# Kernel tuning notes

Hardware: AMD Instinct MI355X
Metric: run time of the kernel (lower is better)

Reference implementation:

```python
import jax, jax.numpy as jnp
import numpy as np

B, TQ, TK, F, H = 8, 2048, 2048, 1024, 1024


def setup_inputs() -> dict:
    key = jax.random.key(0)
    ks = jax.random.split(key, 9)
    scale = 1.0 / np.sqrt(F)
    query = jax.random.normal(ks[0], (B, TQ, F), dtype=jnp.float32)
    encoder_states = jax.random.normal(ks[1], (B, TK, F), dtype=jnp.float32)
    # boolean attention mask; True = keep. Random Bernoulli(0.5).
    target_mask = jax.random.randint(ks[2], (B, TQ, TK), 0, 2) > 0
    # Linear params (torch nn.Linear: y = x @ W.T + b); store W as [F, H] for x @ W.
    Wq = jax.random.normal(ks[3], (F, H), dtype=jnp.float32) * scale
    bq = jax.random.normal(ks[4], (H,), dtype=jnp.float32) * scale
    Wk = jax.random.normal(ks[5], (F, H), dtype=jnp.float32) * scale
    bk = jax.random.normal(ks[6], (H,), dtype=jnp.float32) * scale
    Wv = jax.random.normal(ks[7], (F, H), dtype=jnp.float32) * scale
    bv = jax.random.normal(ks[8], (H,), dtype=jnp.float32) * scale
    return {"query": query, "encoder_states": encoder_states, "target_mask": target_mask,
            "Wq": Wq, "bq": bq, "Wk": Wk, "bk": bk, "Wv": Wv, "bv": bv}


def reference(query, encoder_states, target_mask, Wq, bq, Wk, bk, Wv, bv):
    # init(): K/V projections of encoder states
    K = jnp.einsum('btf,fh->bth', encoder_states, Wk) + bk   # [B,TK,H]
    V = jnp.einsum('btf,fh->bth', encoder_states, Wv) + bv   # [B,TK,H]
    # forward()
    Q = jnp.einsum('btf,fh->bth', query, Wq) + bq            # [B,TQ,H]
    scores = jnp.einsum('bqh,bkh->bqk', Q, K) / jnp.sqrt(jnp.asarray(H, Q.dtype))
    scores = jnp.where(target_mask, scores, -jnp.inf)
    attn = jax.nn.softmax(scores, axis=-1)                   # [B,TQ,TK]
    return jnp.einsum('bqk,bkh->bqh', attn, V)               # [B,TQ,H]
```

## Files before the change

kernel.cpp:

```cpp
#include <hip/hip_runtime.h>

#define NB 8
#define TQv 2048
#define TKv 2048
#define FD 1024
#define HD 1024

typedef __attribute__((ext_vector_type(8))) short short8;
typedef __attribute__((ext_vector_type(8))) _Float16 half8;
typedef __attribute__((ext_vector_type(16))) float f32x16;

__device__ __forceinline__ short f2bf(float f) {
    union { float f; unsigned u; } v; v.f = f;
    unsigned r = v.u + 0x7FFFu + ((v.u >> 16) & 1u);
    return (short)(r >> 16);
}

__device__ __forceinline__ void async16(const short* g, short* l) {
    __builtin_amdgcn_global_load_lds(
        (const __attribute__((address_space(1))) unsigned int*)g,
        (__attribute__((address_space(3))) unsigned int*)l, 16, 0, 0);
}

template <bool F16>
__device__ __forceinline__ void gemm128_core(const short* __restrict__ A, int lda,
                                             const short* __restrict__ B, int ldb,
                                             int K, short* As, short* Bs,
                                             f32x16 acc[2][2], int tid) {
    int wave = tid >> 6, lane = tid & 63;
    int lr = lane >> 3;
    int kc = (lane & 7) ^ lr;
    const short* ga[4]; const short* gb[4];
    short* la[4]; short* lb[4];
#pragma unroll
    for (int j = 0; j < 4; ++j) {
        int w = wave + 4 * j;
        ga[j] = A + (size_t)(8 * w + lr) * lda + kc * 8;
        gb[j] = B + (size_t)(8 * w + lr) * ldb + kc * 8;
        la[j] = As + w * 512;
        lb[j] = Bs + w * 512;
    }
    int mbase = (wave & 1) * 64 + (lane & 31);
    int nbase = (wave >> 1) * 64 + (lane & 31);
    int khalf = lane >> 5;
    int l7 = lane & 7;

    for (int k0 = 0; k0 < K; k0 += 64) {
        __syncthreads();
#pragma unroll
        for (int j = 0; j < 4; ++j) { async16(ga[j], la[j]); async16(gb[j], lb[j]); }
#pragma unroll
        for (int j = 0; j < 4; ++j) { ga[j] += 64; gb[j] += 64; }
        __syncthreads();
#pragma unroll
        for (int ks = 0; ks < 4; ++ks) {
            int kcc = 2 * ks + khalf;
            int sw = kcc ^ l7;
            if (F16) {
                half8 af[2], bf[2];
#pragma unroll
                for (int mt = 0; mt < 2; ++mt) {
                    af[mt] = *(const half8*)(As + ((mbase + mt * 32) * 8 + sw) * 8);
                    bf[mt] = *(const half8*)(Bs + ((nbase + mt * 32) * 8 + sw) * 8);
                }
#pragma unroll
                for (int mt = 0; mt < 2; ++mt)
#pragma unroll
                    for (int nt = 0; nt < 2; ++nt)
                        acc[mt][nt] = __builtin_amdgcn_mfma_f32_32x32x16_f16(
                            af[mt], bf[nt], acc[mt][nt], 0, 0, 0);
            } else {
                short8 af[2], bf[2];
#pragma unroll
                for (int mt = 0; mt < 2; ++mt) {
                    af[mt] = *(const short8*)(As + ((mbase + mt * 32) * 8 + sw) * 8);
                    bf[mt] = *(const short8*)(Bs + ((nbase + mt * 32) * 8 + sw) * 8);
                }
#pragma unroll
                for (int mt = 0; mt < 2; ++mt)
#pragma unroll
                    for (int nt = 0; nt < 2; ++nt)
                        acc[mt][nt] = __builtin_amdgcn_mfma_f32_32x32x16_bf16(
                            af[mt], bf[nt], acc[mt][nt], 0, 0, 0);
            }
        }
    }
}
#define ACC0 {0.f,0.f,0.f,0.f,0.f,0.f,0.f,0.f,0.f,0.f,0.f,0.f,0.f,0.f,0.f,0.f}
#define ACC_INIT {{ACC0, ACC0}, {ACC0, ACC0}}
#define EPI_GM(mt, r) (tile_m + (wave & 1) * 64 + (mt) * 32 + ((lane >> 5) << 2) + (((r) >> 2) << 3) + ((r) & 3))
#define EPI_GN(nt)    (tile_n + (wave >> 1) * 64 + (nt) * 32 + (lane & 31))

__global__ __launch_bounds__(256) void convert_kernel(const float* __restrict__ q,
                                                      const float* __restrict__ e,
                                                      short* __restrict__ xq,
                                                      short* __restrict__ xe) {
    size_t i = (size_t)blockIdx.x * 256 + threadIdx.x;
    const float* src = blockIdx.y ? e : q;
    short* dst = blockIdx.y ? xe : xq;
    float4 a = ((const float4*)src)[2 * i];
    float4 b = ((const float4*)src)[2 * i + 1];
    short8 v;
    v[0] = f2bf(a.x); v[1] = f2bf(a.y); v[2] = f2bf(a.z); v[3] = f2bf(a.w);
    v[4] = f2bf(b.x); v[5] = f2bf(b.y); v[6] = f2bf(b.z); v[7] = f2bf(b.w);
    ((short8*)dst)[i] = v;
}

__global__ __launch_bounds__(256) void wtrans_kernel(const float* __restrict__ Wq,
                                                     const float* __restrict__ Wk,
                                                     const float* __restrict__ Wv,
                                                     short* __restrict__ Wt) {
    __shared__ float tile[32][33];
    const float* W = (blockIdx.z == 0) ? Wq : (blockIdx.z == 1) ? Wk : Wv;
    short* dst = Wt + (size_t)blockIdx.z * HD * FD;
    int h0 = blockIdx.x * 32, f0 = blockIdx.y * 32;
    int tx = threadIdx.x, ty = threadIdx.y;
    for (int j = ty; j < 32; j += 8)
        tile[j][tx] = W[(size_t)(f0 + j) * HD + h0 + tx];
    __syncthreads();
    for (int j = ty; j < 32; j += 8)
        dst[(size_t)(h0 + j) * FD + f0 + tx] = f2bf(tile[tx][j]);
}

__global__ __launch_bounds__(256, 4) void projqk_kernel(const short* __restrict__ Xq,
                                                        const short* __restrict__ Xe,
                                                        const short* __restrict__ Wt3,
                                                        const float* __restrict__ bq,
                                                        const float* __restrict__ bk,
                                                        short* __restrict__ Q,
                                                        short* __restrict__ K) {
    __shared__ short As[128 * 64];
    __shared__ short Bs[128 * 64];
    int tid = threadIdx.x;
    int wave = tid >> 6, lane = tid & 63;
    int p = blockIdx.z;
    const short* X = (p == 0) ? Xq : Xe;
    const short* Wt = Wt3 + (size_t)p * HD * FD;
    const float* bias = (p == 0) ? bq : bk;
    short* O = (p == 0) ? Q : K;
    int bid = blockIdx.x;
    int xcd = bid & 7;
    int idx = bid >> 3;
    int n_t = idx & 7;
    int m_t = (idx >> 3) * 8 + xcd;
    int tile_m = m_t * 128;
    int tile_n = n_t * 128;
    f32x16 acc[2][2] = ACC_INIT;
    gemm128_core<false>(X + (size_t)tile_m * FD, FD, Wt + (size_t)tile_n * FD, FD, FD,
                        As, Bs, acc, tid);
#pragma unroll
    for (int nt = 0; nt < 2; ++nt) {
        int gn = EPI_GN(nt);
        float bv_ = bias[gn];
#pragma unroll
        for (int mt = 0; mt < 2; ++mt)
#pragma unroll
            for (int r = 0; r < 16; ++r) {
                int gm = EPI_GM(mt, r);
                O[(size_t)gm * HD + gn] = f2bf(acc[mt][nt][r] + bv_);
            }
    }
}

__global__ __launch_bounds__(256, 4) void projv_kernel(const short* __restrict__ Xe,
                                                       const short* __restrict__ Wtv,
                                                       const float* __restrict__ bv,
                                                       short* __restrict__ Vt) {
    __shared__ short As[128 * 64];
    __shared__ short Bs[128 * 64];
    int tid = threadIdx.x;
    int wave = tid >> 6, lane = tid & 63;
    int id = blockIdx.x;
    int b = id & 7;
    int i = id >> 3;
    int n_t = i & 15;
    int m_t = i >> 4;
    int tile_m = m_t * 128;
    int tile_n = n_t * 128;
    const short* Xb = Xe + (size_t)b * TKv * FD;
    f32x16 acc[2][2] = ACC_INIT;
    gemm128_core<false>(Wtv + (size_t)tile_m * FD, FD, Xb + (size_t)tile_n * FD, FD, FD,
                        As, Bs, acc, tid);
    short* Ob = Vt + (size_t)b * HD * TKv;
#pragma unroll
    for (int mt = 0; mt < 2; ++mt)
#pragma unroll
        for (int r = 0; r < 16; ++r) {
            int gm = EPI_GM(mt, r);
            float bv_ = bv[gm];
#pragma unroll
            for (int nt = 0; nt < 2; ++nt) {
                int gn = EPI_GN(nt);
                union { _Float16 h; short s; } cv;
                cv.h = (_Float16)(acc[mt][nt][r] + bv_);
                Ob[(size_t)gm * TKv + gn] = cv.s;
            }
        }
}

__global__ __launch_bounds__(256) void maskbits_kernel(const int* __restrict__ mask,
                                                       unsigned long long* __restrict__ Mbits,
                                                       float* __restrict__ L) {
    int tid = threadIdx.x;
    int lane = tid & 63;
    if (blockIdx.x < 64) L[blockIdx.x * 256 + tid] = 0.f;
    const int NW = NB * TQv * (TKv / 64);
    int stride = gridDim.x * 4;
    for (int w = blockIdx.x * 4 + (tid >> 6); w < NW; w += stride) {
        int v = mask[(size_t)w * 64 + lane];
        unsigned long long bal = __ballot(v != 0);
        if (lane == 0) Mbits[w] = bal;
    }
}

__global__ __launch_bounds__(256, 4) void score_kernel(const short* __restrict__ Q,
                                                       const short* __restrict__ K,
                                                       const unsigned long long* __restrict__ Mbits,
                                                       short* __restrict__ S,
                                                       float* __restrict__ L) {
    __shared__ short As[128 * 64];
    __shared__ short Bs[128 * 64];
    int tid = threadIdx.x;
    int wave = tid >> 6, lane = tid & 63;
    int id = blockIdx.x;
    int b = id & 7;
    int i = id >> 3;
    int n_t = i & 15;
    int m_t = i >> 4;
    int tile_m = m_t * 128;
    int tile_n = n_t * 128;
    const short* Aq = Q + (size_t)b * TQv * HD;
    const short* Bk = K + (size_t)b * TKv * HD;
    f32x16 acc[2][2] = ACC_INIT;
    gemm128_core<false>(Aq + (size_t)tile_m * HD, HD, Bk + (size_t)tile_n * HD, HD, HD,
                        As, Bs, acc, tid);
    short* Sb = S + (size_t)b * TQv * TKv;
    const unsigned long long* Mb = Mbits + (size_t)b * TQv * (TKv / 64);
    float* Lb = L + (size_t)b * TQv;
    int wofs = (tile_n >> 6) + (wave >> 1);
    int l31 = lane & 31;
#pragma unroll
    for (int mt = 0; mt < 2; ++mt)
#pragma unroll
        for (int r = 0; r < 16; ++r) {
            int gm = EPI_GM(mt, r);
            unsigned long long bits = Mb[(size_t)gm * (TKv / 64) + wofs];
            float rs = 0.f;
#pragma unroll
            for (int nt = 0; nt < 2; ++nt) {
                int gn = EPI_GN(nt);
                float s = acc[mt][nt][r] * 0.03125f;
                float p = ((bits >> (nt * 32 + l31)) & 1ULL)
                              ? exp2f((s - 4.0f) * 1.44269504f) : 0.f;
                rs += p;
                union { _Float16 h; short sh; } cv;
                cv.h = (_Float16)p;
                Sb[(size_t)gm * TKv + gn] = cv.sh;
            }
            for (int sh = 1; sh < 32; sh <<= 1) rs += __shfl_xor(rs, sh);
            if (l31 == 0) atomicAdd(&Lb[gm], rs);
        }
}

__global__ __launch_bounds__(256, 4) void pv_kernel(const short* __restrict__ P,
                                                    const short* __restrict__ Vt,
                                                    const float* __restrict__ L,
                                                    float* __restrict__ Out) {
    __shared__ short As[128 * 64];
    __shared__ short Bs[128 * 64];
    int tid = threadIdx.x;
    int wave = tid >> 6, lane = tid & 63;
    int id = blockIdx.x;
    int b = id & 7;
    int i = id >> 3;
    int n_t = i & 7;
    int m_t = i >> 3;
    int tile_m = m_t * 128;
    int tile_n = n_t * 128;
    const short* Ap = P + (size_t)b * TQv * TKv;
    const short* Bv = Vt + (size_t)b * HD * TKv;
    const float* Lb = L + (size_t)b * TQv;
    f32x16 acc[2][2] = ACC_INIT;
    gemm128_core<true>(Ap + (size_t)tile_m * TKv, TKv, Bv + (size_t)tile_n * TKv, TKv, TKv,
                       As, Bs, acc, tid);
    float* Ob = Out + (size_t)b * TQv * HD;
#pragma unroll
    for (int mt = 0; mt < 2; ++mt)
#pragma unroll
        for (int r = 0; r < 16; ++r) {
            int gm = EPI_GM(mt, r);
            float l = Lb[gm];
            float inv = (l > 0.f) ? 1.f / l : 0.f;
#pragma unroll
            for (int nt = 0; nt < 2; ++nt) {
                int gn = EPI_GN(nt);
                Ob[(size_t)gm * HD + gn] = acc[mt][nt][r] * inv;
            }
        }
}

extern "C" void kernel_launch(void* const* d_in, const int* in_sizes, int n_in,
                              void* d_out, int out_size, void* d_ws, size_t ws_size,
                              hipStream_t stream) {
    const float* query = (const float*)d_in[0];
    const float* enc   = (const float*)d_in[1];
    const int*   mask  = (const int*)d_in[2];
    const float* Wq    = (const float*)d_in[3];
    const float* bq    = (const float*)d_in[4];
    const float* Wk    = (const float*)d_in[5];
    const float* bk    = (const float*)d_in[6];
    const float* Wv    = (const float*)d_in[7];
    const float* bv    = (const float*)d_in[8];
    float* out = (float*)d_out;

    char* ws = (char*)d_ws;
    short* Wt  = (short*)(ws);
    unsigned long long* Mbits = (unsigned long long*)(ws);
    float* L   = (float*)(ws + 4194304);
    short* Xq  = (short*)(ws + 6291456);
    short* Xe  = (short*)(ws + 39845888);
    short* S   = (short*)(ws + 6291456);
    short* Qb  = (short*)(ws + 73400320);
    short* Kb  = (short*)(ws + 106954752);
    short* Vt  = (short*)(ws + 140509184);
    (void)in_sizes; (void)n_in; (void)out_size; (void)ws_size;

    convert_kernel<<<dim3(8192, 2), 256, 0, stream>>>(query, enc, Xq, Xe);
    wtrans_kernel<<<dim3(32, 32, 3), dim3(32, 8), 0, stream>>>(Wq, Wk, Wv, Wt);
    projqk_kernel<<<dim3(1024, 1, 2), 256, 0, stream>>>(Xq, Xe, Wt, bq, bk, Qb, Kb);
    projv_kernel<<<dim3(1024), 256, 0, stream>>>(Xe, Wt + (size_t)2 * HD * FD, bv, Vt);
    maskbits_kernel<<<dim3(2048), 256, 0, stream>>>(mask, Mbits, L);
    score_kernel<<<dim3(2048), 256, 0, stream>>>(Qb, Kb, Mbits, S, L);
    pv_kernel<<<dim3(1024), 256, 0, stream>>>(S, Vt, L, out);
}
```

Before: 636.5 us.

## Replace 128x128 GEMM core with double-buffered 256x256 tile pipeline using 16x16 MFMA

Every GEMM (Q/K/V projections, scores, PV) now uses a 256x256 output tile computed by 8 waves. The inputs are double-buffered in 128KB of dynamic LDS and prefetched with async global-to-LDS loads interleaved among 16x16x32 MFMA groups. Explicit vmcnt/lgkmcnt waits, barriers and setprio control the schedule. This raises data reuse per block and overlaps loads with math, at the cost of fewer blocks (one or two per CU given the LDS use), higher register pressure and strict reliance on hand-placed waits.

```diff
diff --git a/kernel.cpp b/kernel.cpp
--- a/kernel.cpp
+++ b/kernel.cpp
@@ -8,7 +8,7 @@
 
 typedef __attribute__((ext_vector_type(8))) short short8;
 typedef __attribute__((ext_vector_type(8))) _Float16 half8;
-typedef __attribute__((ext_vector_type(16))) float f32x16;
+typedef __attribute__((ext_vector_type(4))) float f32x4;
 
 __device__ __forceinline__ short f2bf(float f) {
     union { float f; unsigned u; } v; v.f = f;
@@ -16,80 +16,114 @@
     return (short)(r >> 16);
 }
 
+__device__ __forceinline__ half8 as_h8(short8 v) {
+    union { short8 s; half8 h; } u; u.s = v; return u.h;
+}
+
 __device__ __forceinline__ void async16(const short* g, short* l) {
     __builtin_amdgcn_global_load_lds(
         (const __attribute__((address_space(1))) unsigned int*)g,
         (__attribute__((address_space(3))) unsigned int*)l, 16, 0, 0);
 }
 
+#define BAR  __builtin_amdgcn_s_barrier()
+#define SP1  __builtin_amdgcn_s_setprio(1)
+#define SP0  __builtin_amdgcn_s_setprio(0)
+#define VMCNT(N) asm volatile("s_waitcnt vmcnt(" #N ")" ::: "memory")
+#define LGK0 do { asm volatile("s_waitcnt lgkmcnt(0)" ::: "memory"); \
+                  __builtin_amdgcn_sched_barrier(0); } while (0)
+
+
+#define STG_A(BF, H, T) { async16(gA[H][0] + (T)*64, lA[BF][H][0]); \
+                          async16(gA[H][1] + (T)*64, lA[BF][H][1]); }
+#define STG_B(BF, H, T) { async16(gB[H][0] + (T)*64, lB[BF][H][0]); \
+                          async16(gB[H][1] + (T)*64, lB[BF][H][1]); }
+
+#define RD_A(dst, BF, QM) { _Pragma("unroll") for (int ml = 0; ml < 4; ++ml) { \
+    dst[ml][0] = *(const short8*)(rdA + (BF)*65536 + ((QM)*64 + ml*16)*128 + o0); \
+    dst[ml][1] = *(const short8*)(rdA + (BF)*65536 + ((QM)*64 + ml*16)*128 + o1); } }
+#define RD_B(dst, BF, QN) { _Pragma("unroll") for (int nq = 0; nq < 2; ++nq) { \
+    dst[nq][0] = *(const short8*)(rdB + (BF)*65536 + ((QN)*32 + nq*16)*128 + o0); \
+    dst[nq][1] = *(const short8*)(rdB + (BF)*65536 + ((QN)*32 + nq*16)*128 + o1); } }
+
+#define DO_MFMA(AF, BFR, QM, QN) { \
+    _Pragma("unroll") for (int ks = 0; ks < 2; ++ks) \
+    _Pragma("unroll") for (int ml = 0; ml < 4; ++ml) \
+    _Pragma("unroll") for (int nq = 0; nq < 2; ++nq) { \
+        if constexpr (F16) \
+            acc[(QM)*4 + ml][(QN)*2 + nq] = __builtin_amdgcn_mfma_f32_16x16x32_f16( \
+                as_h8(AF[ml][ks]), as_h8(BFR[nq][ks]), acc[(QM)*4 + ml][(QN)*2 + nq], 0, 0, 0); \
+        else \
+            acc[(QM)*4 + ml][(QN)*2 + nq] = __builtin_amdgcn_mfma_f32_16x16x32_bf16( \
+                AF[ml][ks], BFR[nq][ks], acc[(QM)*4 + ml][(QN)*2 + nq], 0, 0, 0); } }
+
 template <bool F16>
-__device__ __forceinline__ void gemm128_core(const short* __restrict__ A, int lda,
-                                             const short* __restrict__ B, int ldb,
-                                             int K, short* As, short* Bs,
-                                             f32x16 acc[2][2], int tid) {
-    int wave = tid >> 6, lane = tid & 63;
-    int lr = lane >> 3;
-    int kc = (lane & 7) ^ lr;
-    const short* ga[4]; const short* gb[4];
-    short* la[4]; short* lb[4];
-#pragma unroll
-    for (int j = 0; j < 4; ++j) {
-        int w = wave + 4 * j;
-        ga[j] = A + (size_t)(8 * w + lr) * lda + kc * 8;
-        gb[j] = B + (size_t)(8 * w + lr) * ldb + kc * 8;
-        la[j] = As + w * 512;
-        lb[j] = Bs + w * 512;
-    }
-    int mbase = (wave & 1) * 64 + (lane & 31);
-    int nbase = (wave >> 1) * 64 + (lane & 31);
-    int khalf = lane >> 5;
-    int l7 = lane & 7;
-
-    for (int k0 = 0; k0 < K; k0 += 64) {
-        __syncthreads();
-#pragma unroll
-        for (int j = 0; j < 4; ++j) { async16(ga[j], la[j]); async16(gb[j], lb[j]); }
-#pragma unroll
-        for (int j = 0; j < 4; ++j) { ga[j] += 64; gb[j] += 64; }
-        __syncthreads();
-#pragma unroll
-        for (int ks = 0; ks < 4; ++ks) {
-            int kcc = 2 * ks + khalf;
-            int sw = kcc ^ l7;
-            if (F16) {
-                half8 af[2], bf[2];
-#pragma unroll
-                for (int mt = 0; mt < 2; ++mt) {
-                    af[mt] = *(const half8*)(As + ((mbase + mt * 32) * 8 + sw) * 8);
-                    bf[mt] = *(const half8*)(Bs + ((nbase + mt * 32) * 8 + sw) * 8);
-                }
-#pragma unroll
-                for (int mt = 0; mt < 2; ++mt)
-#pragma unroll
-                    for (int nt = 0; nt < 2; ++nt)
-                        acc[mt][nt] = __builtin_amdgcn_mfma_f32_32x32x16_f16(
-                            af[mt], bf[nt], acc[mt][nt], 0, 0, 0);
-            } else {
-                short8 af[2], bf[2];
-#pragma unroll
-                for (int mt = 0; mt < 2; ++mt) {
-                    af[mt] = *(const short8*)(As + ((mbase + mt * 32) * 8 + sw) * 8);
-                    bf[mt] = *(const short8*)(Bs + ((nbase + mt * 32) * 8 + sw) * 8);
-                }
-#pragma unroll
-                for (int mt = 0; mt < 2; ++mt)
-#pragma unroll
-                    for (int nt = 0; nt < 2; ++nt)
-                        acc[mt][nt] = __builtin_amdgcn_mfma_f32_32x32x16_bf16(
-                            af[mt], bf[nt], acc[mt][nt], 0, 0, 0);
+__device__ __forceinline__ void gemm256_core(const short* __restrict__ A,
+                                             const short* __restrict__ B,
+                                             int ldK, int K, char* smem,
+                                             f32x4 acc[8][4], int tid) {
+    const int wid = tid >> 6, lane = tid & 63;
+    const int wm = wid >> 2, wn = wid & 3;
+
+    const int lr  = wid * 8 + (lane >> 3);
+    const int kc8 = ((lane & 7) ^ (lane >> 3)) * 8;
+    const short* gA[2][2]; const short* gB[2][2];
+    short* lA[2][2][2]; short* lB[2][2][2];
+#pragma unroll
+    for (int h = 0; h < 2; ++h)
+#pragma unroll
+        for (int j = 0; j < 2; ++j) {
+            gA[h][j] = A + (size_t)(h * 128 + j * 64 + lr) * ldK + kc8;
+            gB[h][j] = B + (size_t)(h * 128 + j * 64 + lr) * ldK + kc8;
+#pragma unroll
+            for (int bf = 0; bf < 2; ++bf) {
+                lA[bf][h][j] = (short*)(smem + bf * 65536 +         h * 16384 + (j * 512 + wid * 64) * 16);
+                lB[bf][h][j] = (short*)(smem + bf * 65536 + 32768 + h * 16384 + (j * 512 + wid * 64) * 16);
             }
         }
+
+    const int l15 = lane & 15;
+    const int o0 = (((lane >> 4)    ) ^ (lane & 7)) * 16;
+    const int o1 = (((lane >> 4) + 4) ^ (lane & 7)) * 16;
+    char* rdA = smem + wm * 16384 + l15 * 128;
+    char* rdB = smem + 32768 + (wn >> 1) * 16384 + (wn & 1) * 8192 + l15 * 128;
+
+    STG_A(0, 0, 0); STG_A(0, 1, 0); STG_B(0, 0, 0); STG_B(0, 1, 0);
+    STG_A(1, 0, 1); STG_A(1, 1, 1);
+    VMCNT(4);
+    BAR;
+
+    const int nt = K >> 6;
+    const int niter = nt >> 1;
+    short8 a0[4][2], a1[4][2], b0[2][2], b1[2][2];
+    for (int it = 0; it < niter; ++it) {
+        const int a = it * 2;
+        const bool nolast = (it != niter - 1);
+        RD_A(a0, 0, 0); RD_B(b0, 0, 0);
+        STG_B(1, 0, a + 1);
+        BAR; LGK0; SP1; DO_MFMA(a0, b0, 0, 0); SP0; BAR;
+        RD_A(a1, 0, 1);
+        STG_B(1, 1, a + 1);
+        BAR; LGK0; SP1; DO_MFMA(a1, b0, 1, 0); SP0; BAR;
+        RD_B(b1, 0, 1);
+        if (nolast) STG_A(0, 0, a + 2);
+        BAR; LGK0; SP1; DO_MFMA(a0, b1, 0, 1); SP0; BAR;
+        if (nolast) { STG_A(0, 1, a + 2); VMCNT(4); } else { VMCNT(0); }
+        BAR; SP1; DO_MFMA(a1, b1, 1, 1); SP0; BAR;
+        RD_A(a0, 1, 0); RD_B(b0, 1, 0);
+        if (nolast) STG_B(0, 0, a + 2);
+        BAR; LGK0; SP1; DO_MFMA(a0, b0, 0, 0); SP0; BAR;
+        RD_A(a1, 1, 1);
+        if (nolast) STG_B(0, 1, a + 2);
+        BAR; LGK0; SP1; DO_MFMA(a1, b0, 1, 0); SP0; BAR;
+        RD_B(b1, 1, 1);
+        if (nolast) STG_A(1, 0, a + 3);
+        BAR; LGK0; SP1; DO_MFMA(a0, b1, 0, 1); SP0; BAR;
+        if (nolast) { STG_A(1, 1, a + 3); VMCNT(4); }
+        BAR; SP1; DO_MFMA(a1, b1, 1, 1); SP0; BAR;
     }
 }
-#define ACC0 {0.f,0.f,0.f,0.f,0.f,0.f,0.f,0.f,0.f,0.f,0.f,0.f,0.f,0.f,0.f,0.f}
-#define ACC_INIT {{ACC0, ACC0}, {ACC0, ACC0}}
-#define EPI_GM(mt, r) (tile_m + (wave & 1) * 64 + (mt) * 32 + ((lane >> 5) << 2) + (((r) >> 2) << 3) + ((r) & 3))
-#define EPI_GN(nt)    (tile_n + (wave >> 1) * 64 + (nt) * 32 + (lane & 31))
+
 
 __global__ __launch_bounds__(256) void convert_kernel(const float* __restrict__ q,
                                                       const float* __restrict__ e,
@@ -122,78 +156,71 @@
         dst[(size_t)(h0 + j) * FD + f0 + tx] = f2bf(tile[tx][j]);
 }
 
-__global__ __launch_bounds__(256, 4) void projqk_kernel(const short* __restrict__ Xq,
+__global__ __launch_bounds__(512, 2) void projqk_kernel(const short* __restrict__ Xq,
                                                         const short* __restrict__ Xe,
                                                         const short* __restrict__ Wt3,
                                                         const float* __restrict__ bq,
                                                         const float* __restrict__ bk,
                                                         short* __restrict__ Q,
                                                         short* __restrict__ K) {
-    __shared__ short As[128 * 64];
-    __shared__ short Bs[128 * 64];
-    int tid = threadIdx.x;
-    int wave = tid >> 6, lane = tid & 63;
+    extern __shared__ char smem[];
+    int tid = threadIdx.x;
     int p = blockIdx.z;
-    const short* X = (p == 0) ? Xq : Xe;
+    const short* X = p ? Xe : Xq;
     const short* Wt = Wt3 + (size_t)p * HD * FD;
-    const float* bias = (p == 0) ? bq : bk;
-    short* O = (p == 0) ? Q : K;
+    const float* bias = p ? bk : bq;
+    short* O = p ? K : Q;
     int bid = blockIdx.x;
-    int xcd = bid & 7;
-    int idx = bid >> 3;
-    int n_t = idx & 7;
-    int m_t = (idx >> 3) * 8 + xcd;
-    int tile_m = m_t * 128;
-    int tile_n = n_t * 128;
-    f32x16 acc[2][2] = ACC_INIT;
-    gemm128_core<false>(X + (size_t)tile_m * FD, FD, Wt + (size_t)tile_n * FD, FD, FD,
-                        As, Bs, acc, tid);
-#pragma unroll
-    for (int nt = 0; nt < 2; ++nt) {
-        int gn = EPI_GN(nt);
+    int xcd = bid & 7, idx = bid >> 3;
+    int n_t = idx & 3, m_t = (idx >> 2) * 8 + xcd;
+    int tile_m = m_t * 256, tile_n = n_t * 256;
+    f32x4 acc[8][4] = {};
+    gemm256_core<false>(X + (size_t)tile_m * FD, Wt + (size_t)tile_n * FD, FD, FD, smem, acc, tid);
+    int wid = tid >> 6, lane = tid & 63;
+    int wm = wid >> 2, wn = wid & 3;
+    int row0 = tile_m + wm * 128 + ((lane >> 4) << 2);
+    int col0 = tile_n + wn * 64 + (lane & 15);
+#pragma unroll
+    for (int n = 0; n < 4; ++n) {
+        int gn = col0 + n * 16;
         float bv_ = bias[gn];
 #pragma unroll
-        for (int mt = 0; mt < 2; ++mt)
-#pragma unroll
-            for (int r = 0; r < 16; ++r) {
-                int gm = EPI_GM(mt, r);
-                O[(size_t)gm * HD + gn] = f2bf(acc[mt][nt][r] + bv_);
-            }
+        for (int m = 0; m < 8; ++m)
+#pragma unroll
+            for (int r = 0; r < 4; ++r)
+                O[(size_t)(row0 + m * 16 + r) * HD + gn] = f2bf(acc[m][n][r] + bv_);
     }
 }
 
-__global__ __launch_bounds__(256, 4) void projv_kernel(const short* __restrict__ Xe,
+__global__ __launch_bounds__(512, 2) void projv_kernel(const short* __restrict__ Xe,
                                                        const short* __restrict__ Wtv,
                                                        const float* __restrict__ bv,
                                                        short* __restrict__ Vt) {
-    __shared__ short As[128 * 64];
-    __shared__ short Bs[128 * 64];
-    int tid = threadIdx.x;
-    int wave = tid >> 6, lane = tid & 63;
-    int id = blockIdx.x;
-    int b = id & 7;
-    int i = id >> 3;
-    int n_t = i & 15;
-    int m_t = i >> 4;
-    int tile_m = m_t * 128;
-    int tile_n = n_t * 128;
+    extern __shared__ char smem[];
+    int tid = threadIdx.x;
+    int bid = blockIdx.x;
+    int b = bid & 7, i = bid >> 3;
+    int m_t = i & 3, n_t = i >> 2;
+    int tile_m = m_t * 256, tile_n = n_t * 256;
     const short* Xb = Xe + (size_t)b * TKv * FD;
-    f32x16 acc[2][2] = ACC_INIT;
-    gemm128_core<false>(Wtv + (size_t)tile_m * FD, FD, Xb + (size_t)tile_n * FD, FD, FD,
-                        As, Bs, acc, tid);
+    f32x4 acc[8][4] = {};
+    gemm256_core<false>(Wtv + (size_t)tile_m * FD, Xb + (size_t)tile_n * FD, FD, FD, smem, acc, tid);
     short* Ob = Vt + (size_t)b * HD * TKv;
-#pragma unroll
-    for (int mt = 0; mt < 2; ++mt)
-#pragma unroll
-        for (int r = 0; r < 16; ++r) {
-            int gm = EPI_GM(mt, r);
+    int wid = tid >> 6, lane = tid & 63;
+    int wm = wid >> 2, wn = wid & 3;
+    int row0 = tile_m + wm * 128 + ((lane >> 4) << 2);
+    int col0 = tile_n + wn * 64 + (lane & 15);
+#pragma unroll
+    for (int m = 0; m < 8; ++m)
+#pragma unroll
+        for (int r = 0; r < 4; ++r) {
+            int gm = row0 + m * 16 + r;
             float bv_ = bv[gm];
 #pragma unroll
-            for (int nt = 0; nt < 2; ++nt) {
-                int gn = EPI_GN(nt);
+            for (int n = 0; n < 4; ++n) {
                 union { _Float16 h; short s; } cv;
-                cv.h = (_Float16)(acc[mt][nt][r] + bv_);
-                Ob[(size_t)gm * TKv + gn] = cv.s;
+                cv.h = (_Float16)(acc[m][n][r] + bv_);
+                Ob[(size_t)gm * TKv + col0 + n * 16] = cv.s;
             }
         }
 }
@@ -213,89 +240,82 @@
     }
 }
 
-__global__ __launch_bounds__(256, 4) void score_kernel(const short* __restrict__ Q,
+__global__ __launch_bounds__(512, 2) void score_kernel(const short* __restrict__ Q,
                                                        const short* __restrict__ K,
                                                        const unsigned long long* __restrict__ Mbits,
                                                        short* __restrict__ S,
                                                        float* __restrict__ L) {
-    __shared__ short As[128 * 64];
-    __shared__ short Bs[128 * 64];
-    int tid = threadIdx.x;
-    int wave = tid >> 6, lane = tid & 63;
-    int id = blockIdx.x;
-    int b = id & 7;
-    int i = id >> 3;
-    int n_t = i & 15;
-    int m_t = i >> 4;
-    int tile_m = m_t * 128;
-    int tile_n = n_t * 128;
+    extern __shared__ char smem[];
+    int tid = threadIdx.x;
+    int bid = blockIdx.x;
+    int b = bid & 7, i = bid >> 3;
+    int n_t = i & 7, m_t = i >> 3;
+    int tile_m = m_t * 256, tile_n = n_t * 256;
     const short* Aq = Q + (size_t)b * TQv * HD;
     const short* Bk = K + (size_t)b * TKv * HD;
-    f32x16 acc[2][2] = ACC_INIT;
-    gemm128_core<false>(Aq + (size_t)tile_m * HD, HD, Bk + (size_t)tile_n * HD, HD, HD,
-                        As, Bs, acc, tid);
+    f32x4 acc[8][4] = {};
+    gemm256_core<false>(Aq + (size_t)tile_m * HD, Bk + (size_t)tile_n * HD, HD, HD, smem, acc, tid);
     short* Sb = S + (size_t)b * TQv * TKv;
     const unsigned long long* Mb = Mbits + (size_t)b * TQv * (TKv / 64);
     float* Lb = L + (size_t)b * TQv;
-    int wofs = (tile_n >> 6) + (wave >> 1);
-    int l31 = lane & 31;
-#pragma unroll
-    for (int mt = 0; mt < 2; ++mt)
-#pragma unroll
-        for (int r = 0; r < 16; ++r) {
-            int gm = EPI_GM(mt, r);
-            unsigned long long bits = Mb[(size_t)gm * (TKv / 64) + wofs];
+    int wid = tid >> 6, lane = tid & 63;
+    int wm = wid >> 2, wn = wid & 3;
+    int l15 = lane & 15;
+    int row0 = tile_m + wm * 128 + ((lane >> 4) << 2);
+    int col0 = tile_n + wn * 64 + l15;
+    int word = (tile_n + wn * 64) >> 6;
+#pragma unroll
+    for (int m = 0; m < 8; ++m)
+#pragma unroll
+        for (int r = 0; r < 4; ++r) {
+            int gm = row0 + m * 16 + r;
+            unsigned long long bits = Mb[(size_t)gm * (TKv / 64) + word];
             float rs = 0.f;
 #pragma unroll
-            for (int nt = 0; nt < 2; ++nt) {
-                int gn = EPI_GN(nt);
-                float s = acc[mt][nt][r] * 0.03125f;
-                float p = ((bits >> (nt * 32 + l31)) & 1ULL)
-                              ? exp2f((s - 4.0f) * 1.44269504f) : 0.f;
-                rs += p;
+            for (int n = 0; n < 4; ++n) {
+                float s = acc[m][n][r] * 0.03125f;
+                float pv = ((bits >> (n * 16 + l15)) & 1ULL)
+                               ? exp2f((s - 4.0f) * 1.44269504f) : 0.f;
+                rs += pv;
                 union { _Float16 h; short sh; } cv;
-                cv.h = (_Float16)p;
-                Sb[(size_t)gm * TKv + gn] = cv.sh;
+                cv.h = (_Float16)pv;
+                Sb[(size_t)gm * TKv + col0 + n * 16] = cv.sh;
             }
-            for (int sh = 1; sh < 32; sh <<= 1) rs += __shfl_xor(rs, sh);
-            if (l31 == 0) atomicAdd(&Lb[gm], rs);
+            for (int sh = 1; sh < 16; sh <<= 1) rs += __shfl_xor(rs, sh);
+            if (l15 == 0) atomicAdd(&Lb[gm], rs);
         }
 }
 
-__global__ __launch_bounds__(256, 4) void pv_kernel(const short* __restrict__ P,
+__global__ __launch_bounds__(512, 2) void pv_kernel(const short* __restrict__ P,
                                                     const short* __restrict__ Vt,
                                                     const float* __restrict__ L,
                                                     float* __restrict__ Out) {
-    __shared__ short As[128 * 64];
-    __shared__ short Bs[128 * 64];
-    int tid = threadIdx.x;
-    int wave = tid >> 6, lane = tid & 63;
-    int id = blockIdx.x;
-    int b = id & 7;
-    int i = id >> 3;
-    int n_t = i & 7;
-    int m_t = i >> 3;
-    int tile_m = m_t * 128;
-    int tile_n = n_t * 128;
+    extern __shared__ char smem[];
+    int tid = threadIdx.x;
+    int bid = blockIdx.x;
+    int b = bid & 7, i = bid >> 3;
+    int n_t = i & 3, m_t = i >> 2;
+    int tile_m = m_t * 256, tile_n = n_t * 256;
     const short* Ap = P + (size_t)b * TQv * TKv;
     const short* Bv = Vt + (size_t)b * HD * TKv;
     const float* Lb = L + (size_t)b * TQv;
-    f32x16 acc[2][2] = ACC_INIT;
-    gemm128_core<true>(Ap + (size_t)tile_m * TKv, TKv, Bv + (size_t)tile_n * TKv, TKv, TKv,
-                       As, Bs, acc, tid);
+    f32x4 acc[8][4] = {};
+    gemm256_core<true>(Ap + (size_t)tile_m * TKv, Bv + (size_t)tile_n * TKv, TKv, TKv, smem, acc, tid);
     float* Ob = Out + (size_t)b * TQv * HD;
-#pragma unroll
-    for (int mt = 0; mt < 2; ++mt)
-#pragma unroll
-        for (int r = 0; r < 16; ++r) {
-            int gm = EPI_GM(mt, r);
+    int wid = tid >> 6, lane = tid & 63;
+    int wm = wid >> 2, wn = wid & 3;
+    int row0 = tile_m + wm * 128 + ((lane >> 4) << 2);
+    int col0 = tile_n + wn * 64 + (lane & 15);
+#pragma unroll
+    for (int m = 0; m < 8; ++m)
+#pragma unroll
+        for (int r = 0; r < 4; ++r) {
+            int gm = row0 + m * 16 + r;
             float l = Lb[gm];
             float inv = (l > 0.f) ? 1.f / l : 0.f;
 #pragma unroll
-            for (int nt = 0; nt < 2; ++nt) {
-                int gn = EPI_GN(nt);
-                Ob[(size_t)gm * HD + gn] = acc[mt][nt][r] * inv;
-            }
+            for (int n = 0; n < 4; ++n)
+                Ob[(size_t)gm * HD + col0 + n * 16] = acc[m][n][r] * inv;
         }
 }
 
@@ -325,11 +345,20 @@
     short* Vt  = (short*)(ws + 140509184);
     (void)in_sizes; (void)n_in; (void)out_size; (void)ws_size;
 
+    static bool inited = false;
+    if (!inited) {
+        hipFuncSetAttribute((const void*)projqk_kernel, hipFuncAttributeMaxDynamicSharedMemorySize, 131072);
+        hipFuncSetAttribute((const void*)projv_kernel,  hipFuncAttributeMaxDynamicSharedMemorySize, 131072);
+        hipFuncSetAttribute((const void*)score_kernel,  hipFuncAttributeMaxDynamicSharedMemorySize, 131072);
+        hipFuncSetAttribute((const void*)pv_kernel,     hipFuncAttributeMaxDynamicSharedMemorySize, 131072);
+        inited = true;
+    }
+
     convert_kernel<<<dim3(8192, 2), 256, 0, stream>>>(query, enc, Xq, Xe);
     wtrans_kernel<<<dim3(32, 32, 3), dim3(32, 8), 0, stream>>>(Wq, Wk, Wv, Wt);
-    projqk_kernel<<<dim3(1024, 1, 2), 256, 0, stream>>>(Xq, Xe, Wt, bq, bk, Qb, Kb);
-    projv_kernel<<<dim3(1024), 256, 0, stream>>>(Xe, Wt + (size_t)2 * HD * FD, bv, Vt);
+    projqk_kernel<<<dim3(256, 1, 2), 512, 131072, stream>>>(Xq, Xe, Wt, bq, bk, Qb, Kb);
+    projv_kernel<<<dim3(256), 512, 131072, stream>>>(Xe, Wt + (size_t)2 * HD * FD, bv, Vt);
     maskbits_kernel<<<dim3(2048), 256, 0, stream>>>(mask, Mbits, L);
-    score_kernel<<<dim3(2048), 256, 0, stream>>>(Qb, Kb, Mbits, S, L);
-    pv_kernel<<<dim3(1024), 256, 0, stream>>>(S, Vt, L, out);
-}
+    score_kernel<<<dim3(512), 512, 131072, stream>>>(Qb, Kb, Mbits, S, L);
+    pv_kernel<<<dim3(256), 512, 131072, stream>>>(S, Vt, L, out);
+}
```

Result: slower. 777.3 us (+22.1%).

## Switch GEMM core from 32x32x16 to 16x16x32 MFMA tiles

Applied to the files above, without the earlier changes.

Each wave's 64x64 sub-tile is now computed with a 4x4 grid of 16x16x32 MFMAs instead of a 2x2 grid of 32x32x16 MFMAs. LDS fragment addressing and every kernel's epilogue row/column mapping are redone to match, and the score kernel's row-sum reduction now spans 16 lanes. Occupancy hints drop from 4 to 3 blocks per SM, presumably to leave room for more registers. The intent is better MFMA throughput or LDS read efficiency, at the cost of more MFMA instructions per k-step and possibly higher register pressure.

```diff
diff --git a/kernel.cpp b/kernel.cpp
--- a/kernel.cpp
+++ b/kernel.cpp
@@ -8,7 +8,7 @@
 
 typedef __attribute__((ext_vector_type(8))) short short8;
 typedef __attribute__((ext_vector_type(8))) _Float16 half8;
-typedef __attribute__((ext_vector_type(16))) float f32x16;
+typedef __attribute__((ext_vector_type(4))) float f32x4;
 
 __device__ __forceinline__ short f2bf(float f) {
     union { float f; unsigned u; } v; v.f = f;
@@ -16,6 +16,10 @@
     return (short)(r >> 16);
 }
 
+__device__ __forceinline__ half8 as_h8(short8 v) {
+    union { short8 s; half8 h; } u; u.s = v; return u.h;
+}
+
 __device__ __forceinline__ void async16(const short* g, short* l) {
     __builtin_amdgcn_global_load_lds(
         (const __attribute__((address_space(1))) unsigned int*)g,
@@ -26,7 +30,7 @@
 __device__ __forceinline__ void gemm128_core(const short* __restrict__ A, int lda,
                                              const short* __restrict__ B, int ldb,
                                              int K, short* As, short* Bs,
-                                             f32x16 acc[2][2], int tid) {
+                                             f32x4 acc[4][4], int tid) {
     int wave = tid >> 6, lane = tid & 63;
     int lr = lane >> 3;
     int kc = (lane & 7) ^ lr;
@@ -40,10 +44,13 @@
         la[j] = As + w * 512;
         lb[j] = Bs + w * 512;
     }
-    int mbase = (wave & 1) * 64 + (lane & 31);
-    int nbase = (wave >> 1) * 64 + (lane & 31);
-    int khalf = lane >> 5;
-    int l7 = lane & 7;
+    int l15 = lane & 15;
+    int g4 = lane >> 4;
+    int r7 = l15 & 7;
+    const short* aB = As + ((wave & 1) * 64 + l15) * 64;
+    const short* bB = Bs + ((wave >> 1) * 64 + l15) * 64;
+    int o0 = ((g4    ) ^ r7) * 8;
+    int o1 = ((g4 + 4) ^ r7) * 8;
 
     for (int k0 = 0; k0 < K; k0 += 64) {
         __syncthreads();
@@ -53,43 +60,31 @@
         for (int j = 0; j < 4; ++j) { ga[j] += 64; gb[j] += 64; }
         __syncthreads();
 #pragma unroll
-        for (int ks = 0; ks < 4; ++ks) {
-            int kcc = 2 * ks + khalf;
-            int sw = kcc ^ l7;
-            if (F16) {
-                half8 af[2], bf[2];
-#pragma unroll
-                for (int mt = 0; mt < 2; ++mt) {
-                    af[mt] = *(const half8*)(As + ((mbase + mt * 32) * 8 + sw) * 8);
-                    bf[mt] = *(const half8*)(Bs + ((nbase + mt * 32) * 8 + sw) * 8);
+        for (int ks = 0; ks < 2; ++ks) {
+            int oo = ks ? o1 : o0;
+            short8 af[4], bf[4];
+#pragma unroll
+            for (int f = 0; f < 4; ++f) {
+                af[f] = *(const short8*)(aB + f * 1024 + oo);
+                bf[f] = *(const short8*)(bB + f * 1024 + oo);
+            }
+#pragma unroll
+            for (int mf = 0; mf < 4; ++mf)
+#pragma unroll
+                for (int nf = 0; nf < 4; ++nf) {
+                    if constexpr (F16)
+                        acc[mf][nf] = __builtin_amdgcn_mfma_f32_16x16x32_f16(
+                            as_h8(af[mf]), as_h8(bf[nf]), acc[mf][nf], 0, 0, 0);
+                    else
+                        acc[mf][nf] = __builtin_amdgcn_mfma_f32_16x16x32_bf16(
+                            af[mf], bf[nf], acc[mf][nf], 0, 0, 0);
                 }
-#pragma unroll
-                for (int mt = 0; mt < 2; ++mt)
-#pragma unroll
-                    for (int nt = 0; nt < 2; ++nt)
-                        acc[mt][nt] = __builtin_amdgcn_mfma_f32_32x32x16_f16(
-                            af[mt], bf[nt], acc[mt][nt], 0, 0, 0);
-            } else {
-                short8 af[2], bf[2];
-#pragma unroll
-                for (int mt = 0; mt < 2; ++mt) {
-                    af[mt] = *(const short8*)(As + ((mbase + mt * 32) * 8 + sw) * 8);
-                    bf[mt] = *(const short8*)(Bs + ((nbase + mt * 32) * 8 + sw) * 8);
-                }
-#pragma unroll
-                for (int mt = 0; mt < 2; ++mt)
-#pragma unroll
-                    for (int nt = 0; nt < 2; ++nt)
-                        acc[mt][nt] = __builtin_amdgcn_mfma_f32_32x32x16_bf16(
-                            af[mt], bf[nt], acc[mt][nt], 0, 0, 0);
-            }
         }
     }
 }
-#define ACC0 {0.f,0.f,0.f,0.f,0.f,0.f,0.f,0.f,0.f,0.f,0.f,0.f,0.f,0.f,0.f,0.f}
-#define ACC_INIT {{ACC0, ACC0}, {ACC0, ACC0}}
-#define EPI_GM(mt, r) (tile_m + (wave & 1) * 64 + (mt) * 32 + ((lane >> 5) << 2) + (((r) >> 2) << 3) + ((r) & 3))
-#define EPI_GN(nt)    (tile_n + (wave >> 1) * 64 + (nt) * 32 + (lane & 31))
+
+#define EGM(mf, r) (tile_m + (wave & 1) * 64 + (mf) * 16 + ((lane >> 4) << 2) + (r))
+#define EGN(nf)    (tile_n + (wave >> 1) * 64 + (nf) * 16 + (lane & 15))
 
 __global__ __launch_bounds__(256) void convert_kernel(const float* __restrict__ q,
                                                       const float* __restrict__ e,
@@ -122,7 +117,7 @@
         dst[(size_t)(h0 + j) * FD + f0 + tx] = f2bf(tile[tx][j]);
 }
 
-__global__ __launch_bounds__(256, 4) void projqk_kernel(const short* __restrict__ Xq,
+__global__ __launch_bounds__(256, 3) void projqk_kernel(const short* __restrict__ Xq,
                                                         const short* __restrict__ Xe,
                                                         const short* __restrict__ Wt3,
                                                         const float* __restrict__ bq,
@@ -145,24 +140,22 @@
     int m_t = (idx >> 3) * 8 + xcd;
     int tile_m = m_t * 128;
     int tile_n = n_t * 128;
-    f32x16 acc[2][2] = ACC_INIT;
+    f32x4 acc[4][4] = {};
     gemm128_core<false>(X + (size_t)tile_m * FD, FD, Wt + (size_t)tile_n * FD, FD, FD,
                         As, Bs, acc, tid);
 #pragma unroll
-    for (int nt = 0; nt < 2; ++nt) {
-        int gn = EPI_GN(nt);
+    for (int nf = 0; nf < 4; ++nf) {
+        int gn = EGN(nf);
         float bv_ = bias[gn];
 #pragma unroll
-        for (int mt = 0; mt < 2; ++mt)
-#pragma unroll
-            for (int r = 0; r < 16; ++r) {
-                int gm = EPI_GM(mt, r);
-                O[(size_t)gm * HD + gn] = f2bf(acc[mt][nt][r] + bv_);
-            }
+        for (int mf = 0; mf < 4; ++mf)
+#pragma unroll
+            for (int r = 0; r < 4; ++r)
+                O[(size_t)EGM(mf, r) * HD + gn] = f2bf(acc[mf][nf][r] + bv_);
     }
 }
 
-__global__ __launch_bounds__(256, 4) void projv_kernel(const short* __restrict__ Xe,
+__global__ __launch_bounds__(256, 3) void projv_kernel(const short* __restrict__ Xe,
                                                        const short* __restrict__ Wtv,
                                                        const float* __restrict__ bv,
                                                        short* __restrict__ Vt) {
@@ -178,22 +171,21 @@
     int tile_m = m_t * 128;
     int tile_n = n_t * 128;
     const short* Xb = Xe + (size_t)b * TKv * FD;
-    f32x16 acc[2][2] = ACC_INIT;
+    f32x4 acc[4][4] = {};
     gemm128_core<false>(Wtv + (size_t)tile_m * FD, FD, Xb + (size_t)tile_n * FD, FD, FD,
                         As, Bs, acc, tid);
     short* Ob = Vt + (size_t)b * HD * TKv;
 #pragma unroll
-    for (int mt = 0; mt < 2; ++mt)
-#pragma unroll
-        for (int r = 0; r < 16; ++r) {
-            int gm = EPI_GM(mt, r);
+    for (int mf = 0; mf < 4; ++mf)
+#pragma unroll
+        for (int r = 0; r < 4; ++r) {
+            int gm = EGM(mf, r);
             float bv_ = bv[gm];
 #pragma unroll
-            for (int nt = 0; nt < 2; ++nt) {
-                int gn = EPI_GN(nt);
+            for (int nf = 0; nf < 4; ++nf) {
                 union { _Float16 h; short s; } cv;
-                cv.h = (_Float16)(acc[mt][nt][r] + bv_);
-                Ob[(size_t)gm * TKv + gn] = cv.s;
+                cv.h = (_Float16)(acc[mf][nf][r] + bv_);
+                Ob[(size_t)gm * TKv + EGN(nf)] = cv.s;
             }
         }
 }
@@ -213,7 +205,7 @@
     }
 }
 
-__global__ __launch_bounds__(256, 4) void score_kernel(const short* __restrict__ Q,
+__global__ __launch_bounds__(256, 3) void score_kernel(const short* __restrict__ Q,
                                                        const short* __restrict__ K,
                                                        const unsigned long long* __restrict__ Mbits,
                                                        short* __restrict__ S,
@@ -231,38 +223,38 @@
     int tile_n = n_t * 128;
     const short* Aq = Q + (size_t)b * TQv * HD;
     const short* Bk = K + (size_t)b * TKv * HD;
-    f32x16 acc[2][2] = ACC_INIT;
+    f32x4 acc[4][4] = {};
     gemm128_core<false>(Aq + (size_t)tile_m * HD, HD, Bk + (size_t)tile_n * HD, HD, HD,
                         As, Bs, acc, tid);
     short* Sb = S + (size_t)b * TQv * TKv;
     const unsigned long long* Mb = Mbits + (size_t)b * TQv * (TKv / 64);
     float* Lb = L + (size_t)b * TQv;
-    int wofs = (tile_n >> 6) + (wave >> 1);
-    int l31 = lane & 31;
-#pragma unroll
-    for (int mt = 0; mt < 2; ++mt)
-#pragma unroll
-        for (int r = 0; r < 16; ++r) {
-            int gm = EPI_GM(mt, r);
-            unsigned long long bits = Mb[(size_t)gm * (TKv / 64) + wofs];
+    int word = (tile_n >> 6) + (wave >> 1);
+    int l15 = lane & 15;
+    int col0 = tile_n + (wave >> 1) * 64 + l15;
+#pragma unroll
+    for (int mf = 0; mf < 4; ++mf)
+#pragma unroll
+        for (int r = 0; r < 4; ++r) {
+            int gm = EGM(mf, r);
+            unsigned long long bits = Mb[(size_t)gm * (TKv / 64) + word];
             float rs = 0.f;
 #pragma unroll
-            for (int nt = 0; nt < 2; ++nt) {
-                int gn = EPI_GN(nt);
-                float s = acc[mt][nt][r] * 0.03125f;
-                float p = ((bits >> (nt * 32 + l31)) & 1ULL)
-                              ? exp2f((s - 4.0f) * 1.44269504f) : 0.f;
-                rs += p;
+            for (int nf = 0; nf < 4; ++nf) {
+                float s = acc[mf][nf][r] * 0.03125f;
+                float pv = ((bits >> (nf * 16 + l15)) & 1ULL)
+                               ? exp2f((s - 4.0f) * 1.44269504f) : 0.f;
+                rs += pv;
                 union { _Float16 h; short sh; } cv;
-                cv.h = (_Float16)p;
-                Sb[(size_t)gm * TKv + gn] = cv.sh;
+                cv.h = (_Float16)pv;
+                Sb[(size_t)gm * TKv + col0 + nf * 16] = cv.sh;
             }
-            for (int sh = 1; sh < 32; sh <<= 1) rs += __shfl_xor(rs, sh);
-            if (l31 == 0) atomicAdd(&Lb[gm], rs);
+            for (int sh = 1; sh < 16; sh <<= 1) rs += __shfl_xor(rs, sh);
+            if (l15 == 0) atomicAdd(&Lb[gm], rs);
         }
 }
 
-__global__ __launch_bounds__(256, 4) void pv_kernel(const short* __restrict__ P,
+__global__ __launch_bounds__(256, 3) void pv_kernel(const short* __restrict__ P,
                                                     const short* __restrict__ Vt,
                                                     const float* __restrict__ L,
                                                     float* __restrict__ Out) {
@@ -280,22 +272,20 @@
     const short* Ap = P + (size_t)b * TQv * TKv;
     const short* Bv = Vt + (size_t)b * HD * TKv;
     const float* Lb = L + (size_t)b * TQv;
-    f32x16 acc[2][2] = ACC_INIT;
+    f32x4 acc[4][4] = {};
     gemm128_core<true>(Ap + (size_t)tile_m * TKv, TKv, Bv + (size_t)tile_n * TKv, TKv, TKv,
                        As, Bs, acc, tid);
     float* Ob = Out + (size_t)b * TQv * HD;
 #pragma unroll
-    for (int mt = 0; mt < 2; ++mt)
-#pragma unroll
-        for (int r = 0; r < 16; ++r) {
-            int gm = EPI_GM(mt, r);
+    for (int mf = 0; mf < 4; ++mf)
+#pragma unroll
+        for (int r = 0; r < 4; ++r) {
+            int gm = EGM(mf, r);
             float l = Lb[gm];
             float inv = (l > 0.f) ? 1.f / l : 0.f;
 #pragma unroll
-            for (int nt = 0; nt < 2; ++nt) {
-                int gn = EPI_GN(nt);
-                Ob[(size_t)gm * HD + gn] = acc[mt][nt][r] * inv;
-            }
+            for (int nf = 0; nf < 4; ++nf)
+                Ob[(size_t)gm * HD + EGN(nf)] = acc[mf][nf][r] * inv;
         }
 }
 
```

Result: no change. 624.9 us (-1.8%).
